# Optimization experiments

Measured on AMD Instinct MI355X. Metric: run time of the kernel, lower is better.

The kernel has to match this reference:

```python
import math
import jax, jax.numpy as jnp
import numpy as np

N_NODES = 50_000
N_EDGES = 500_000
INPUT_DIM = 6
HIDDEN = 128
FREQS = 32
LN_EPS = 1e-5
TWO_PI = 2.0 * math.pi


def wrap_angle(a):
    return (a + math.pi) % (2.0 * math.pi) - math.pi


def setup_inputs() -> dict:
    key = jax.random.key(0)
    ks = jax.random.split(key, 12)
    source = jax.random.normal(ks[0], (N_NODES, 5), dtype=jnp.float32)
    target = jax.random.normal(ks[1], (N_NODES, 5), dtype=jnp.float32)
    edge = jax.random.randint(ks[2], (2, N_EDGES), 0, N_NODES, dtype=jnp.int64)
    K = 2 * FREQS + 1
    # FourierEmbedding params: freqs table + 6 per-dim MLPs (Linear->LN->ReLU->Linear), stacked over dim axis
    freqs = jax.random.normal(ks[3], (INPUT_DIM, FREQS), dtype=jnp.float32)
    W1 = jax.random.normal(ks[4], (INPUT_DIM, K, HIDDEN), dtype=jnp.float32) * (1.0 / math.sqrt(K))
    b1 = jnp.zeros((INPUT_DIM, HIDDEN), dtype=jnp.float32)
    ln_w = jnp.ones((INPUT_DIM, HIDDEN), dtype=jnp.float32)
    ln_b = jnp.zeros((INPUT_DIM, HIDDEN), dtype=jnp.float32)
    W2 = jax.random.normal(ks[5], (INPUT_DIM, HIDDEN, HIDDEN), dtype=jnp.float32) * (1.0 / math.sqrt(HIDDEN))
    b2 = jnp.zeros((INPUT_DIM, HIDDEN), dtype=jnp.float32)
    return {"source": source, "target": target, "edge": edge,
            "freqs": freqs, "W1": W1, "b1": b1, "ln_w": ln_w, "ln_b": ln_b,
            "W2": W2, "b2": b2}


def _compute_feature(source, target, edge):
    # source/target: [N, 5] = X, Y, Heading, Speed, (other)
    sp, sh, ss = source[:, :2], source[:, 2], source[:, 3]
    tp, th, ts = target[:, :2], target[:, 2], target[:, 3]
    src, tgt = edge[0], edge[1]
    pd = sp[src] - tp[tgt]                         # [E, 2]
    dx, dy = pd[:, 0], pd[:, 1]
    dist = jnp.sqrt(dx * dx + dy * dy)
    is_close = (dist < 3.0).astype(pd.dtype)
    ang = jnp.arctan2(dy, dx)
    dh = wrap_angle(sh[src] - th[tgt])
    cos_a, sin_a = jnp.cos(ang), jnp.sin(ang)
    tvx, tvy = ts * jnp.cos(th), ts * jnp.sin(th)
    t_close = tvx[tgt] * cos_a + tvy[tgt] * sin_a
    svx, svy = ss * jnp.cos(sh), ss * jnp.sin(sh)
    s_close = svx[src] * cos_a + svy[src] * sin_a
    return jnp.stack([dx, dy, dh, is_close, t_close, s_close], axis=-1)  # [E, 6]


def _fourier_embed(feat, freqs, W1, b1, ln_w, ln_b, W2, b2):
    # feat: [E, 6]; freqs: [6, F]
    x = feat[:, :, None] * freqs[None, :, :] * TWO_PI          # [E, 6, F]
    x = jnp.concatenate([jnp.cos(x), jnp.sin(x), feat[:, :, None]], axis=-1)  # [E, 6, 2F+1]
    h = jnp.einsum('edk,dkh->edh', x, W1) + b1[None]           # [E, 6, H]
    mu = h.mean(axis=-1, keepdims=True)
    var = jnp.mean((h - mu) ** 2, axis=-1, keepdims=True)
    h = (h - mu) * jax.lax.rsqrt(var + LN_EPS) * ln_w[None] + ln_b[None]
    h = jax.nn.relu(h)
    out = jnp.einsum('edh,dhg->edg', h, W2) + b2[None]         # [E, 6, H]
    return out.sum(axis=1)                                     # [E, H]


def reference(source, target, edge, freqs, W1, b1, ln_w, ln_b, W2, b2):
    feat = jax.lax.stop_gradient(_compute_feature(source, target, edge))  # torch.no_grad()
    return _fourier_embed(feat, freqs, W1, b1, ln_w, ln_b, W2, b2)
```

## Files before the change

kernel.cpp:

```cpp
#include <hip/hip_runtime.h>
#include <hip/hip_bf16.h>
#include <math.h>

#define E_EDGES 500000
#define PI_F 3.14159265358979323846f
#define TWOPI_F 6.28318530717958647692f

typedef __attribute__((ext_vector_type(4))) float f32x4;
typedef __attribute__((ext_vector_type(8))) short s16x8;

static __device__ __forceinline__ short f2bf(float x) {
    __hip_bfloat16 h = __float2bfloat16(x);
    return __builtin_bit_cast(short, h);
}

__global__ __launch_bounds__(256, 2)
void rape_mfma_kernel(const float* __restrict__ source,
                      const float* __restrict__ target,
                      const int*   __restrict__ edge,
                      const float* __restrict__ freqs,
                      const float* __restrict__ W1,
                      const float* __restrict__ b1,
                      const float* __restrict__ ln_w,
                      const float* __restrict__ ln_b,
                      const float* __restrict__ W2,
                      const float* __restrict__ b2,
                      float* __restrict__ out)
{
    __shared__ s16x8 w1t[12 * 128];
    __shared__ s16x8 w2t[16 * 128];
    __shared__ float feat_s[6][128];
    __shared__ float freq_s[6 * 32];
    __shared__ float b1_s[6 * 128];
    __shared__ float lnw_s[6 * 128];
    __shared__ float lnb_s[6 * 128];

    const int tid   = threadIdx.x;
    const int lane  = tid & 63;
    const int wv    = tid >> 6;
    const int c     = lane & 15;
    const int g     = lane >> 4;
    const int half  = tid >> 7;
    const int ebase = blockIdx.x * 128;

    if (tid < 128) {
        int ec = ebase + tid; if (ec >= E_EDGES) ec = E_EDGES - 1;
        int si = edge[ec];
        int ti = edge[E_EDGES + ec];
        const float* S = source + (size_t)si * 5;
        const float* T = target + (size_t)ti * 5;
        float spx = S[0], spy = S[1], shd = S[2], ss = S[3];
        float tpx = T[0], tpy = T[1], thd = T[2], ts = T[3];
        float dx = spx - tpx, dy = spy - tpy;
        float dist = sqrtf(dx * dx + dy * dy);
        float ic  = dist < 3.0f ? 1.0f : 0.0f;
        float inv = dist > 0.0f ? 1.0f / dist : 0.0f;
        float ca  = dist > 0.0f ? dx * inv : 1.0f;
        float sa  = dy * inv;
        float a = shd - thd + PI_F;
        float r = fmodf(a, TWOPI_F);
        r = r < 0.0f ? r + TWOPI_F : r;
        float dh = r - PI_F;
        float tc = ts * (cosf(thd) * ca + sinf(thd) * sa);
        float sc = ss * (cosf(shd) * ca + sinf(shd) * sa);
        feat_s[0][tid] = dx; feat_s[1][tid] = dy; feat_s[2][tid] = dh;
        feat_s[3][tid] = ic; feat_s[4][tid] = tc; feat_s[5][tid] = sc;
    }
    if (tid < 192) freq_s[tid] = freqs[tid];
    for (int i = tid; i < 768; i += 256) {
        b1_s[i] = b1[i]; lnw_s[i] = ln_w[i]; lnb_s[i] = ln_b[i];
    }
    {
        s16x8 z = {0, 0, 0, 0, 0, 0, 0, 0};
        for (int i = tid; i < 3 * 128; i += 256) w1t[9 * 128 + i] = z;
    }

    f32x4 acc[2][8];
    #pragma unroll
    for (int gt = 0; gt < 8; ++gt) {
        f32x4 s = {0.f, 0.f, 0.f, 0.f};
        #pragma unroll
        for (int d = 0; d < 6; ++d) {
            const f32x4 v = *(const f32x4*)(b2 + d * 128 + gt * 16 + g * 4);
            s += v;
        }
        acc[0][gt] = s; acc[1][gt] = s;
    }

    for (int d = 0; d < 6; ++d) {
        __syncthreads();

        {
            const int j = tid & 127;
            const float* W1d = W1 + (size_t)d * 65 * 128;
            #pragma unroll
            for (int it = 0; it < 4; ++it) {
                const int sg = half + it * 2;
                const int kb = (sg >> 2) * 32 + (sg & 3) * 4;
                s16x8 v;
                #pragma unroll
                for (int i = 0; i < 4; ++i) {
                    v[i]     = f2bf(W1d[(kb + i) * 128 + j]);
                    v[i + 4] = f2bf(W1d[(kb + 16 + i) * 128 + j]);
                }
                w1t[sg * 128 + j] = v;
            }
            if (half == 0) {
                s16x8 v = {0, 0, 0, 0, 0, 0, 0, 0};
                v[0] = f2bf(W1d[64 * 128 + j]);
                w1t[8 * 128 + j] = v;
            }
            const float* W2d = W2 + (size_t)d * 128 * 128;
            #pragma unroll
            for (int it = 0; it < 8; ++it) {
                const int sg = half + it * 2;
                const int kb = (sg >> 2) * 32 + (sg & 3) * 4;
                s16x8 v;
                #pragma unroll
                for (int i = 0; i < 4; ++i) {
                    v[i]     = f2bf(W2d[(kb + i) * 128 + j]);
                    v[i + 4] = f2bf(W2d[(kb + 16 + i) * 128 + j]);
                }
                w2t[sg * 128 + j] = v;
            }
        }
        __syncthreads();

        s16x8 bfr[2][3];
        #pragma unroll
        for (int es = 0; es < 2; ++es) {
            const float x = feat_s[d][wv * 32 + es * 16 + c];
            const f32x4 fq0 = *(const f32x4*)(freq_s + d * 32 + g * 4);
            const f32x4 fq1 = *(const f32x4*)(freq_s + d * 32 + 16 + g * 4);
            s16x8 bc, bs;
            #pragma unroll
            for (int i = 0; i < 8; ++i) {
                const float f = (i < 4) ? fq0[i] : fq1[i - 4];
                const float t = x * f;
                const float tf = t - floorf(t);
                bc[i] = f2bf(__builtin_amdgcn_cosf(tf));
                bs[i] = f2bf(__builtin_amdgcn_sinf(tf));
            }
            s16x8 bx = {0, 0, 0, 0, 0, 0, 0, 0};
            if (g == 0) bx[0] = f2bf(x);
            bfr[es][0] = bc; bfr[es][1] = bs; bfr[es][2] = bx;
        }

        f32x4 d1[2][8];
        #pragma unroll
        for (int jt = 0; jt < 8; ++jt) {
            const f32x4 bv = *(const f32x4*)(b1_s + d * 128 + jt * 16 + g * 4);
            d1[0][jt] = bv; d1[1][jt] = bv;
        }
        #pragma unroll
        for (int jt = 0; jt < 8; ++jt) {
            const s16x8 a0 = w1t[(0 + g) * 128 + jt * 16 + c];
            const s16x8 a1 = w1t[(4 + g) * 128 + jt * 16 + c];
            const s16x8 a2 = w1t[(8 + g) * 128 + jt * 16 + c];
            #pragma unroll
            for (int es = 0; es < 2; ++es) {
                d1[es][jt] = __builtin_amdgcn_mfma_f32_16x16x32_bf16(a0, bfr[es][0], d1[es][jt], 0, 0, 0);
                d1[es][jt] = __builtin_amdgcn_mfma_f32_16x16x32_bf16(a1, bfr[es][1], d1[es][jt], 0, 0, 0);
                d1[es][jt] = __builtin_amdgcn_mfma_f32_16x16x32_bf16(a2, bfr[es][2], d1[es][jt], 0, 0, 0);
            }
        }

        s16x8 pb[2][4];
        #pragma unroll
        for (int es = 0; es < 2; ++es) {
            float s1 = 0.f, s2 = 0.f;
            #pragma unroll
            for (int jt = 0; jt < 8; ++jt)
                #pragma unroll
                for (int q = 0; q < 4; ++q) {
                    const float v = d1[es][jt][q];
                    s1 += v; s2 = fmaf(v, v, s2);
                }
            s1 += __shfl_xor(s1, 16); s1 += __shfl_xor(s1, 32);
            s2 += __shfl_xor(s2, 16); s2 += __shfl_xor(s2, 32);
            const float mu   = s1 * 0.0078125f;
            const float var  = s2 * 0.0078125f - mu * mu;
            const float rinv = rsqrtf(var + 1e-5f);
            #pragma unroll
            for (int ks = 0; ks < 4; ++ks) {
                #pragma unroll
                for (int p = 0; p < 2; ++p) {
                    const int jt = 2 * ks + p;
                    const f32x4 lw = *(const f32x4*)(lnw_s + d * 128 + jt * 16 + g * 4);
                    const f32x4 lb = *(const f32x4*)(lnb_s + d * 128 + jt * 16 + g * 4);
                    #pragma unroll
                    for (int q = 0; q < 4; ++q) {
                        float hv = (d1[es][jt][q] - mu) * rinv;
                        hv = fmaf(hv, lw[q], lb[q]);
                        hv = fmaxf(hv, 0.f);
                        pb[es][ks][q + 4 * p] = f2bf(hv);
                    }
                }
            }
        }

        #pragma unroll
        for (int gt = 0; gt < 8; ++gt) {
            const s16x8 a0 = w2t[(0 * 4 + g) * 128 + gt * 16 + c];
            const s16x8 a1 = w2t[(1 * 4 + g) * 128 + gt * 16 + c];
            const s16x8 a2 = w2t[(2 * 4 + g) * 128 + gt * 16 + c];
            const s16x8 a3 = w2t[(3 * 4 + g) * 128 + gt * 16 + c];
            #pragma unroll
            for (int es = 0; es < 2; ++es) {
                acc[es][gt] = __builtin_amdgcn_mfma_f32_16x16x32_bf16(a0, pb[es][0], acc[es][gt], 0, 0, 0);
                acc[es][gt] = __builtin_amdgcn_mfma_f32_16x16x32_bf16(a1, pb[es][1], acc[es][gt], 0, 0, 0);
                acc[es][gt] = __builtin_amdgcn_mfma_f32_16x16x32_bf16(a2, pb[es][2], acc[es][gt], 0, 0, 0);
                acc[es][gt] = __builtin_amdgcn_mfma_f32_16x16x32_bf16(a3, pb[es][3], acc[es][gt], 0, 0, 0);
            }
        }
    }

    #pragma unroll
    for (int es = 0; es < 2; ++es) {
        const int e = ebase + wv * 32 + es * 16 + c;
        if (e < E_EDGES) {
            float* op = out + (size_t)e * 128 + g * 4;
            #pragma unroll
            for (int gt = 0; gt < 8; ++gt)
                *(f32x4*)(op + gt * 16) = acc[es][gt];
        }
    }
}

extern "C" void kernel_launch(void* const* d_in, const int* in_sizes, int n_in,
                              void* d_out, int out_size, void* d_ws, size_t ws_size,
                              hipStream_t stream) {
    const float* source = (const float*)d_in[0];
    const float* target = (const float*)d_in[1];
    const int*   edge   = (const int*)  d_in[2];
    const float* freqs  = (const float*)d_in[3];
    const float* W1     = (const float*)d_in[4];
    const float* b1     = (const float*)d_in[5];
    const float* ln_w   = (const float*)d_in[6];
    const float* ln_b   = (const float*)d_in[7];
    const float* W2     = (const float*)d_in[8];
    const float* b2     = (const float*)d_in[9];
    float* out = (float*)d_out;

    const int nblocks = (E_EDGES + 127) / 128;
    rape_mfma_kernel<<<nblocks, 256, 0, stream>>>(
        source, target, edge, freqs, W1, b1, ln_w, ln_b, W2, b2, out);
}
```

Measured before the change: 284.9 us.

## Pre-convert weights to bf16 in a prep kernel and DMA them into LDS

A separate prep kernel converts W1/W2 to bf16 in the MFMA-friendly layout once per call into workspace. The main kernel then copies each dimension's slab straight into LDS with global_load_lds, which removes the per-block fp32 loads and conversions. The 65th W1 row is now applied as an fp32 rank-1 update, dropping one MFMA per tile. Small parameters are read from global memory instead of staged in LDS, LDS use shrinks, and occupancy is raised to 3 blocks. This adds an extra kernel launch and makes the main kernel depend on uncached global reads of the small parameter vectors.

```diff
diff --git a/kernel.cpp b/kernel.cpp
--- a/kernel.cpp
+++ b/kernel.cpp
@@ -14,33 +14,56 @@
     return __builtin_bit_cast(short, h);
 }
 
-__global__ __launch_bounds__(256, 2)
-void rape_mfma_kernel(const float* __restrict__ source,
-                      const float* __restrict__ target,
-                      const int*   __restrict__ edge,
-                      const float* __restrict__ freqs,
-                      const float* __restrict__ W1,
-                      const float* __restrict__ b1,
-                      const float* __restrict__ ln_w,
-                      const float* __restrict__ ln_b,
-                      const float* __restrict__ W2,
-                      const float* __restrict__ b2,
-                      float* __restrict__ out)
+__global__ void rape_prep_kernel(const float* __restrict__ W1,
+                                 const float* __restrict__ W2,
+                                 s16x8* __restrict__ ws)
 {
-    __shared__ s16x8 w1t[12 * 128];
-    __shared__ s16x8 w2t[16 * 128];
+    const int d  = blockIdx.x / 24;
+    const int sg = blockIdx.x % 24;
+    const int j  = threadIdx.x;
+    s16x8 v;
+    if (sg < 8) {
+        const float* W1d = W1 + (size_t)d * 65 * 128;
+        const int kb = (sg >> 2) * 32 + (sg & 3) * 4;
+        #pragma unroll
+        for (int i = 0; i < 4; ++i) {
+            v[i]     = f2bf(W1d[(kb + i) * 128 + j]);
+            v[i + 4] = f2bf(W1d[(kb + 16 + i) * 128 + j]);
+        }
+    } else {
+        const int sg2 = sg - 8;
+        const float* W2d = W2 + (size_t)d * 128 * 128;
+        const int kb = (sg2 >> 2) * 32 + (sg2 & 3) * 4;
+        #pragma unroll
+        for (int i = 0; i < 4; ++i) {
+            v[i]     = f2bf(W2d[(kb + i) * 128 + j]);
+            v[i + 4] = f2bf(W2d[(kb + 16 + i) * 128 + j]);
+        }
+    }
+    ws[(size_t)d * 24 * 128 + sg * 128 + j] = v;
+}
+
+__global__ __launch_bounds__(256, 3)
+void rape_mfma2_kernel(const float* __restrict__ source,
+                       const float* __restrict__ target,
+                       const int*   __restrict__ edge,
+                       const float* __restrict__ freqs,
+                       const float* __restrict__ W1,
+                       const float* __restrict__ b1,
+                       const float* __restrict__ ln_w,
+                       const float* __restrict__ ln_b,
+                       const float* __restrict__ b2,
+                       const s16x8* __restrict__ wsg,
+                       float* __restrict__ out)
+{
+    __shared__ s16x8 slab[24 * 128];
     __shared__ float feat_s[6][128];
-    __shared__ float freq_s[6 * 32];
-    __shared__ float b1_s[6 * 128];
-    __shared__ float lnw_s[6 * 128];
-    __shared__ float lnb_s[6 * 128];
 
     const int tid   = threadIdx.x;
     const int lane  = tid & 63;
     const int wv    = tid >> 6;
     const int c     = lane & 15;
     const int g     = lane >> 4;
-    const int half  = tid >> 7;
     const int ebase = blockIdx.x * 128;
 
     if (tid < 128) {
@@ -66,24 +89,14 @@
         feat_s[0][tid] = dx; feat_s[1][tid] = dy; feat_s[2][tid] = dh;
         feat_s[3][tid] = ic; feat_s[4][tid] = tc; feat_s[5][tid] = sc;
     }
-    if (tid < 192) freq_s[tid] = freqs[tid];
-    for (int i = tid; i < 768; i += 256) {
-        b1_s[i] = b1[i]; lnw_s[i] = ln_w[i]; lnb_s[i] = ln_b[i];
-    }
-    {
-        s16x8 z = {0, 0, 0, 0, 0, 0, 0, 0};
-        for (int i = tid; i < 3 * 128; i += 256) w1t[9 * 128 + i] = z;
-    }
 
     f32x4 acc[2][8];
     #pragma unroll
     for (int gt = 0; gt < 8; ++gt) {
         f32x4 s = {0.f, 0.f, 0.f, 0.f};
         #pragma unroll
-        for (int d = 0; d < 6; ++d) {
-            const f32x4 v = *(const f32x4*)(b2 + d * 128 + gt * 16 + g * 4);
-            s += v;
-        }
+        for (int d = 0; d < 6; ++d)
+            s += *(const f32x4*)(b2 + d * 128 + gt * 16 + g * 4);
         acc[0][gt] = s; acc[1][gt] = s;
     }
 
@@ -91,47 +104,25 @@
         __syncthreads();
 
         {
-            const int j = tid & 127;
-            const float* W1d = W1 + (size_t)d * 65 * 128;
-            #pragma unroll
-            for (int it = 0; it < 4; ++it) {
-                const int sg = half + it * 2;
-                const int kb = (sg >> 2) * 32 + (sg & 3) * 4;
-                s16x8 v;
-                #pragma unroll
-                for (int i = 0; i < 4; ++i) {
-                    v[i]     = f2bf(W1d[(kb + i) * 128 + j]);
-                    v[i + 4] = f2bf(W1d[(kb + 16 + i) * 128 + j]);
-                }
-                w1t[sg * 128 + j] = v;
-            }
-            if (half == 0) {
-                s16x8 v = {0, 0, 0, 0, 0, 0, 0, 0};
-                v[0] = f2bf(W1d[64 * 128 + j]);
-                w1t[8 * 128 + j] = v;
-            }
-            const float* W2d = W2 + (size_t)d * 128 * 128;
-            #pragma unroll
-            for (int it = 0; it < 8; ++it) {
-                const int sg = half + it * 2;
-                const int kb = (sg >> 2) * 32 + (sg & 3) * 4;
-                s16x8 v;
-                #pragma unroll
-                for (int i = 0; i < 4; ++i) {
-                    v[i]     = f2bf(W2d[(kb + i) * 128 + j]);
-                    v[i + 4] = f2bf(W2d[(kb + 16 + i) * 128 + j]);
-                }
-                w2t[sg * 128 + j] = v;
-            }
-        }
-        __syncthreads();
-
-        s16x8 bfr[2][3];
+            const char* gsrc = (const char*)(wsg + (size_t)d * 24 * 128);
+            #pragma unroll
+            for (int it = 0; it < 12; ++it) {
+                const int off = tid * 16 + it * 4096;
+                __builtin_amdgcn_global_load_lds(
+                    (const __attribute__((address_space(1))) unsigned int*)(gsrc + off),
+                    (__attribute__((address_space(3))) unsigned int*)((char*)slab + off),
+                    16, 0, 0);
+            }
+        }
+
+        s16x8 bfr[2][2];
+        float xv[2];
         #pragma unroll
         for (int es = 0; es < 2; ++es) {
             const float x = feat_s[d][wv * 32 + es * 16 + c];
-            const f32x4 fq0 = *(const f32x4*)(freq_s + d * 32 + g * 4);
-            const f32x4 fq1 = *(const f32x4*)(freq_s + d * 32 + 16 + g * 4);
+            xv[es] = x;
+            const f32x4 fq0 = *(const f32x4*)(freqs + d * 32 + g * 4);
+            const f32x4 fq1 = *(const f32x4*)(freqs + d * 32 + 16 + g * 4);
             s16x8 bc, bs;
             #pragma unroll
             for (int i = 0; i < 8; ++i) {
@@ -141,27 +132,31 @@
                 bc[i] = f2bf(__builtin_amdgcn_cosf(tf));
                 bs[i] = f2bf(__builtin_amdgcn_sinf(tf));
             }
-            s16x8 bx = {0, 0, 0, 0, 0, 0, 0, 0};
-            if (g == 0) bx[0] = f2bf(x);
-            bfr[es][0] = bc; bfr[es][1] = bs; bfr[es][2] = bx;
+            bfr[es][0] = bc; bfr[es][1] = bs;
         }
 
         f32x4 d1[2][8];
+        {
+            const float* w164 = W1 + ((size_t)d * 65 + 64) * 128;
+            #pragma unroll
+            for (int jt = 0; jt < 8; ++jt) {
+                const f32x4 bv = *(const f32x4*)(b1 + d * 128 + jt * 16 + g * 4);
+                const f32x4 wv4 = *(const f32x4*)(w164 + jt * 16 + g * 4);
+                d1[0][jt] = bv + xv[0] * wv4;
+                d1[1][jt] = bv + xv[1] * wv4;
+            }
+        }
+
+        __syncthreads();
+
         #pragma unroll
         for (int jt = 0; jt < 8; ++jt) {
-            const f32x4 bv = *(const f32x4*)(b1_s + d * 128 + jt * 16 + g * 4);
-            d1[0][jt] = bv; d1[1][jt] = bv;
-        }
-        #pragma unroll
-        for (int jt = 0; jt < 8; ++jt) {
-            const s16x8 a0 = w1t[(0 + g) * 128 + jt * 16 + c];
-            const s16x8 a1 = w1t[(4 + g) * 128 + jt * 16 + c];
-            const s16x8 a2 = w1t[(8 + g) * 128 + jt * 16 + c];
+            const s16x8 a0 = slab[(0 + g) * 128 + jt * 16 + c];
+            const s16x8 a1 = slab[(4 + g) * 128 + jt * 16 + c];
             #pragma unroll
             for (int es = 0; es < 2; ++es) {
                 d1[es][jt] = __builtin_amdgcn_mfma_f32_16x16x32_bf16(a0, bfr[es][0], d1[es][jt], 0, 0, 0);
                 d1[es][jt] = __builtin_amdgcn_mfma_f32_16x16x32_bf16(a1, bfr[es][1], d1[es][jt], 0, 0, 0);
-                d1[es][jt] = __builtin_amdgcn_mfma_f32_16x16x32_bf16(a2, bfr[es][2], d1[es][jt], 0, 0, 0);
             }
         }
 
@@ -186,8 +181,8 @@
                 #pragma unroll
                 for (int p = 0; p < 2; ++p) {
                     const int jt = 2 * ks + p;
-                    const f32x4 lw = *(const f32x4*)(lnw_s + d * 128 + jt * 16 + g * 4);
-                    const f32x4 lb = *(const f32x4*)(lnb_s + d * 128 + jt * 16 + g * 4);
+                    const f32x4 lw = *(const f32x4*)(ln_w + d * 128 + jt * 16 + g * 4);
+                    const f32x4 lb = *(const f32x4*)(ln_b + d * 128 + jt * 16 + g * 4);
                     #pragma unroll
                     for (int q = 0; q < 4; ++q) {
                         float hv = (d1[es][jt][q] - mu) * rinv;
@@ -201,10 +196,10 @@
 
         #pragma unroll
         for (int gt = 0; gt < 8; ++gt) {
-            const s16x8 a0 = w2t[(0 * 4 + g) * 128 + gt * 16 + c];
-            const s16x8 a1 = w2t[(1 * 4 + g) * 128 + gt * 16 + c];
-            const s16x8 a2 = w2t[(2 * 4 + g) * 128 + gt * 16 + c];
-            const s16x8 a3 = w2t[(3 * 4 + g) * 128 + gt * 16 + c];
+            const s16x8 a0 = slab[(8 + 0 * 4 + g) * 128 + gt * 16 + c];
+            const s16x8 a1 = slab[(8 + 1 * 4 + g) * 128 + gt * 16 + c];
+            const s16x8 a2 = slab[(8 + 2 * 4 + g) * 128 + gt * 16 + c];
+            const s16x8 a3 = slab[(8 + 3 * 4 + g) * 128 + gt * 16 + c];
             #pragma unroll
             for (int es = 0; es < 2; ++es) {
                 acc[es][gt] = __builtin_amdgcn_mfma_f32_16x16x32_bf16(a0, pb[es][0], acc[es][gt], 0, 0, 0);
@@ -241,8 +236,11 @@
     const float* W2     = (const float*)d_in[8];
     const float* b2     = (const float*)d_in[9];
     float* out = (float*)d_out;
+    s16x8* wsg = (s16x8*)d_ws;
+
+    rape_prep_kernel<<<6 * 24, 128, 0, stream>>>(W1, W2, wsg);
 
     const int nblocks = (E_EDGES + 127) / 128;
-    rape_mfma_kernel<<<nblocks, 256, 0, stream>>>(
-        source, target, edge, freqs, W1, b1, ln_w, ln_b, W2, b2, out);
-}
+    rape_mfma2_kernel<<<nblocks, 256, 0, stream>>>(
+        source, target, edge, freqs, W1, b1, ln_w, ln_b, b2, wsg, out);
+}
```

After: 326.2 us. 1.15x slower.
